# Kernel tuning notes

Measured on AMD Instinct MI355X. Metric: run time of the kernel, lower is better.

The kernel has to match this reference:

```python
import jax, jax.numpy as jnp
import numpy as np

B, C, N, M = 4, 256, 4096, 4096
H, D = 4, 64  # num_heads, head_dim = C // H


def _proj(x, W, b):
    # Conv1d(kernel_size=1): pointwise linear over channel dim. x:(B,Cin,L) W:(Cout,Cin) b:(Cout,)
    return jnp.einsum('oc,bcn->bon', W, x) + b[None, :, None]


def setup_inputs() -> dict:
    key = jax.random.key(0)
    ks = jax.random.split(key, 10)
    s = 1.0 / np.sqrt(C)
    return {
        'query': jax.random.normal(ks[0], (B, C, N), dtype=jnp.float32),
        'source': jax.random.normal(ks[1], (B, C, M), dtype=jnp.float32),
        'Wq': jax.random.normal(ks[2], (C, C), dtype=jnp.float32) * s,
        'bq': jnp.zeros((C,), dtype=jnp.float32),
        'Wk': jax.random.normal(ks[3], (C, C), dtype=jnp.float32) * s,
        'bk': jnp.zeros((C,), dtype=jnp.float32),
        'Wv': jax.random.normal(ks[4], (C, C), dtype=jnp.float32) * s,
        'bv': jnp.zeros((C,), dtype=jnp.float32),
        'Wm': jax.random.normal(ks[5], (C, C), dtype=jnp.float32) * s,
        'bm': jnp.zeros((C,), dtype=jnp.float32),
    }


def reference(query, source, Wq, bq, Wk, bk, Wv, bv, Wm, bm):
    b = query.shape[0]
    n = query.shape[-1]
    Q = _proj(query, Wq, bq).reshape(b, H, D, -1)   # (B,H,D,N)
    K = _proj(source, Wk, bk).reshape(b, H, D, -1)  # (B,H,D,M)
    V = _proj(source, Wv, bv).reshape(b, H, D, -1)  # (B,H,D,M)
    scores = jnp.einsum('bhdn,bhdm->bhnm', Q, K) / (D ** 0.5)
    attn = jax.nn.softmax(scores, axis=-1)
    out = jnp.einsum('bhnm,bhdm->bhdn', attn, V)    # (B,H,D,N)
    out = out.reshape(b, H * D, n)                   # (B,C,N)
    return _proj(out, Wm, bm)
```

## Files before the change

### kernel.cpp

```cpp
#include <hip/hip_runtime.h>
#include <hip/hip_bf16.h>
#include <stdint.h>

#define BB 4
#define CCH 256
#define NN 4096
#define MM 4096
#define HH 4
#define DDIM 64

typedef __attribute__((ext_vector_type(8))) short short8v;
typedef __attribute__((ext_vector_type(4))) float f32x4;
typedef __attribute__((ext_vector_type(16))) float f32x16;

__device__ __forceinline__ unsigned short f2b(float f) {
    unsigned int u = __builtin_bit_cast(unsigned int, f);
    unsigned int r = (u + 0x7FFFu + ((u >> 16) & 1u)) >> 16;
    return (unsigned short)r;
}

__device__ __forceinline__ f32x16 zero16() {
    f32x16 z;
#pragma unroll
    for (int i = 0; i < 16; i++) z[i] = 0.f;
    return z;
}

__global__ __launch_bounds__(256) void convert_kernel(
    const float* __restrict__ q, const float* __restrict__ s,
    const float* __restrict__ Wq, const float* __restrict__ Wk,
    const float* __restrict__ Wv, const float* __restrict__ Wm,
    unsigned short* __restrict__ XTq, unsigned short* __restrict__ XTs,
    unsigned short* __restrict__ Wb) {
    __shared__ float tile[64][65];
    const int bid = blockIdx.x, tid = threadIdx.x;
    if (bid < 2048) {
        const float* in = (bid < 1024) ? q : s;
        unsigned short* out = (bid < 1024) ? XTq : XTs;
        const int r = bid & 1023;
        const int b = r >> 8;
        const int rr = r & 255;
        const int l0 = (rr >> 2) * 64, c0 = (rr & 3) * 64;
#pragma unroll
        for (int i = 0; i < 16; i++) {
            int idx = tid + (i << 8);
            int cc = idx >> 6, ll = idx & 63;
            tile[cc][ll] = in[(size_t)(b * CCH + c0 + cc) * 4096 + l0 + ll];
        }
        __syncthreads();
#pragma unroll
        for (int i = 0; i < 16; i++) {
            int idx = tid + (i << 8);
            int ll = idx >> 6, cc = idx & 63;
            out[((size_t)(b * 4096 + l0 + ll) << 8) + c0 + cc] = f2b(tile[cc][ll]);
        }
    } else {
        const int wid = bid - 2048;
        const int wsel = wid >> 4;
        const float* src = (wsel == 0) ? Wq : (wsel == 1) ? Wk : (wsel == 2) ? Wv : Wm;
        const int off = (wid & 15) * 4096;
#pragma unroll
        for (int i = 0; i < 16; i++) {
            int idx = off + tid + (i << 8);
            Wb[(size_t)wsel * 65536 + idx] = f2b(src[idx]);
        }
    }
}

template <int OUTMODE, bool AHEAD>
__device__ __forceinline__ void gemm_body(const unsigned short* __restrict__ XT,
                                          const unsigned short* __restrict__ W,
                                          const float* __restrict__ bias,
                                          void* __restrict__ outv, float oscale) {
    constexpr int WSTR = 264;
    constexpr int XSTR = 40;
    __shared__ __align__(16) unsigned short Wlds[64 * WSTR];
    __shared__ __align__(16) unsigned short Xlds[256 * XSTR];
    const int tid = threadIdx.x, w = tid >> 6, l = tid & 63;
    const int lg = l >> 4, lm = l & 15;
    const int n0 = blockIdx.x * 256, o0 = blockIdx.y * 64;
    const int oh = (w >> 1) * 32, nh = (w & 1) * 128;

#pragma unroll
    for (int i = 0; i < 8; i++) {
        int idx = tid + (i << 8);
        int row = idx >> 5, c8 = (idx & 31) * 8;
        *(uint4*)&Wlds[row * WSTR + c8] = *(const uint4*)&W[(size_t)(o0 + row) * 256 + c8];
    }

    f32x4 acc[8][2];
#pragma unroll
    for (int nt = 0; nt < 8; nt++)
#pragma unroll
        for (int ot = 0; ot < 2; ot++) acc[nt][ot] = (f32x4){0.f, 0.f, 0.f, 0.f};

    for (int kc = 0; kc < 8; kc++) {
#pragma unroll
        for (int i = 0; i < 4; i++) {
            int idx = tid + (i << 8);
            int row = idx >> 2;
            const unsigned short* srcp;
            if constexpr (AHEAD) {
                int c = kc * 32 + (idx & 3) * 8;
                srcp = XT + ((size_t)(c >> 6) * 4096 + n0 + row) * 64 + (c & 63);
            } else {
                srcp = XT + (size_t)(n0 + row) * 256 + kc * 32 + (idx & 3) * 8;
            }
            *(uint4*)&Xlds[row * XSTR + (idx & 3) * 8] = *(const uint4*)srcp;
        }
        __syncthreads();
        short8v bfrag[2];
#pragma unroll
        for (int ot = 0; ot < 2; ot++)
            bfrag[ot] = *(const short8v*)&Wlds[(oh + ot * 16 + lm) * WSTR + kc * 32 + lg * 8];
#pragma unroll
        for (int nt = 0; nt < 8; nt++) {
            short8v af = *(const short8v*)&Xlds[(nh + nt * 16 + lm) * XSTR + lg * 8];
            acc[nt][0] = __builtin_amdgcn_mfma_f32_16x16x32_bf16(af, bfrag[0], acc[nt][0], 0, 0, 0);
            acc[nt][1] = __builtin_amdgcn_mfma_f32_16x16x32_bf16(af, bfrag[1], acc[nt][1], 0, 0, 0);
        }
        __syncthreads();
    }

#pragma unroll
    for (int nt = 0; nt < 8; nt++)
#pragma unroll
        for (int ot = 0; ot < 2; ot++) {
            int o = o0 + oh + ot * 16 + lm;
            int nb = n0 + nh + nt * 16 + lg * 4;
            float bb = bias[o];
            if constexpr (OUTMODE == 2) {
                float* out = (float*)outv;
                float4 v = make_float4(acc[nt][ot][0] + bb, acc[nt][ot][1] + bb,
                                       acc[nt][ot][2] + bb, acc[nt][ot][3] + bb);
                *(float4*)&out[(size_t)o * 4096 + nb] = v;
            } else if constexpr (OUTMODE == 0) {
                unsigned short* out = (unsigned short*)outv;
                __align__(8) unsigned short v[4];
#pragma unroll
                for (int t = 0; t < 4; t++) v[t] = f2b(acc[nt][ot][t] + bb);
                *(uint2*)&out[(size_t)o * 4096 + nb] = *(uint2*)v;
            } else {
                unsigned short* out = (unsigned short*)outv;
                unsigned short* outp = out + ((size_t)(o >> 6) * 4096 + nb) * 64 + (o & 63);
#pragma unroll
                for (int t = 0; t < 4; t++) outp[t * 64] = f2b((acc[nt][ot][t] + bb) * oscale);
            }
        }
}

__global__ __launch_bounds__(256) void gemm_qkv_kernel(
    const unsigned short* __restrict__ XTq, const unsigned short* __restrict__ XTs,
    const unsigned short* __restrict__ Wb,
    const float* __restrict__ bq, const float* __restrict__ bk, const float* __restrict__ bv,
    unsigned short* __restrict__ QT, unsigned short* __restrict__ KT,
    unsigned short* __restrict__ Vn) {
    const int z = blockIdx.z;
    const int b = z / 3, p = z - b * 3;
    const unsigned short* XT = ((p == 0) ? XTq : XTs) + (size_t)b * 4096 * 256;
    const unsigned short* W = Wb + p * 65536;
    const float* bias = (p == 0) ? bq : (p == 1) ? bk : bv;
    if (p == 2) {
        gemm_body<0, false>(XT, W, bias, Vn + (size_t)b * 256 * 4096, 1.0f);
    } else {
        unsigned short* out = ((p == 0) ? QT : KT) + (size_t)b * 1048576;
        gemm_body<1, false>(XT, W, bias, out, (p == 0) ? 0.1803368801f : 1.0f);
    }
}

__global__ __launch_bounds__(256) void gemm_final_kernel(
    const unsigned short* __restrict__ OH, const unsigned short* __restrict__ Wm,
    const float* __restrict__ bm, float* __restrict__ out) {
    const int b = blockIdx.z;
    gemm_body<2, true>(OH + (size_t)b * 1048576, Wm, bm, out + (size_t)b * 256 * 4096, 1.0f);
}

__device__ __forceinline__ void stage_kv(const unsigned short* __restrict__ Kb,
                                         const unsigned short* __restrict__ Vb,
                                         char* dst, int m0s, int tid) {
    const int rr = tid >> 3, pp = tid & 7;
    const int sw = (pp ^ (rr & 7)) << 4;
    const char* sK = (const char*)(Kb + ((size_t)(m0s + rr) << 6)) + sw;
    const char* sV = (const char*)(Vb + (size_t)rr * 4096 + m0s) + sw;
    __builtin_amdgcn_global_load_lds(
        (const __attribute__((address_space(1))) unsigned int*)sK,
        (__attribute__((address_space(3))) unsigned int*)(dst + (tid << 4)), 16, 0, 0);
    __builtin_amdgcn_global_load_lds(
        (const __attribute__((address_space(1))) unsigned int*)sV,
        (__attribute__((address_space(3))) unsigned int*)(dst + 8192 + (tid << 4)), 16, 0, 0);
}

__global__ __launch_bounds__(512, 2) void attn_kernel(
    const unsigned short* __restrict__ QT, const unsigned short* __restrict__ KT,
    const unsigned short* __restrict__ Vn, unsigned short* __restrict__ OH) {
    __shared__ __align__(16) char smem[32768];
    const int tid = threadIdx.x, w = tid >> 6, l = tid & 63;
    const int lo5 = l & 31, hi = l >> 5;
    const int bh = blockIdx.y, b = bh >> 2, h = bh & 3;
    const int q0 = blockIdx.x * 256 + w * 32;

    short8v qf[4];
    {
        size_t qrow = ((size_t)bh * 4096 + q0 + lo5) * 64;
#pragma unroll
        for (int c = 0; c < 4; c++)
            qf[c] = *(const short8v*)&QT[qrow + c * 16 + hi * 8];
    }

    short8v ones;
#pragma unroll
    for (int j = 0; j < 8; j++) ones[j] = (short)0x3F80;
    f32x16 minit;
#pragma unroll
    for (int r = 0; r < 16; r++) minit[r] = -16.0f;

    const unsigned short* Vb = Vn + ((size_t)b * 256 + h * 64) * 4096;
    const unsigned short* Kb = KT + (size_t)bh * 262144;

    f32x16 o[2];
    o[0] = zero16();
    o[1] = zero16();
    f32x16 sacc = zero16();

    stage_kv(Kb, Vb, smem, 0, tid);

    for (int it = 0; it < 64; it++) {
        __syncthreads();
        char* cur = smem + ((it & 1) << 14);
        if (it < 63) stage_kv(Kb, Vb, smem + (((it + 1) & 1) << 14), (it + 1) * 64, tid);

        short8v kf[2][4];
#pragma unroll
        for (int mc = 0; mc < 2; mc++) {
            int m = mc * 32 + lo5;
#pragma unroll
            for (int c = 0; c < 4; c++)
                kf[mc][c] = *(const short8v*)(cur + m * 128 + (((c * 2 + hi) * 16) ^ ((m & 7) << 4)));
        }
        short8v vf[2][4];
#pragma unroll
        for (int dc = 0; dc < 2; dc++) {
            int d = dc * 32 + lo5;
#pragma unroll
            for (int c = 0; c < 4; c++)
                vf[dc][c] = *(const short8v*)(cur + 8192 + d * 128 + (((c * 2 + hi) * 16) ^ ((d & 7) << 4)));
        }

        f32x16 s[2];
#pragma unroll
        for (int mc = 0; mc < 2; mc++) {
            f32x16 a = __builtin_amdgcn_mfma_f32_32x32x16_bf16(kf[mc][0], qf[0], minit, 0, 0, 0);
#pragma unroll
            for (int c = 1; c < 4; c++)
                a = __builtin_amdgcn_mfma_f32_32x32x16_bf16(kf[mc][c], qf[c], a, 0, 0, 0);
            s[mc] = a;
        }

        short8v pv[2][2];
#pragma unroll
        for (int mc = 0; mc < 2; mc++) {
            float p[16];
#pragma unroll
            for (int r = 0; r < 16; r++) p[r] = exp2f(s[mc][r]);
#pragma unroll
            for (int half = 0; half < 2; half++) {
                union { unsigned int u[4]; short8v v; } pu;
#pragma unroll
                for (int wdx = 0; wdx < 2; wdx++) {
                    unsigned int a, bq;
                    asm("v_cvt_pk_bf16_f32 %0, %1, %2"
                        : "=v"(a) : "v"(p[half * 8 + 2 * wdx]), "v"(p[half * 8 + 2 * wdx + 1]));
                    asm("v_cvt_pk_bf16_f32 %0, %1, %2"
                        : "=v"(bq) : "v"(p[half * 8 + 4 + 2 * wdx]), "v"(p[half * 8 + 4 + 2 * wdx + 1]));
                    asm volatile("v_permlane32_swap_b32 %0, %1" : "+v"(a), "+v"(bq));
                    pu.u[wdx] = a;
                    pu.u[wdx + 2] = bq;
                }
                pv[mc][half] = pu.v;
            }
        }

#pragma unroll
        for (int mc = 0; mc < 2; mc++)
#pragma unroll
            for (int half = 0; half < 2; half++)
                sacc = __builtin_amdgcn_mfma_f32_32x32x16_bf16(ones, pv[mc][half], sacc, 0, 0, 0);

#pragma unroll
        for (int dc = 0; dc < 2; dc++)
#pragma unroll
            for (int mc = 0; mc < 2; mc++)
#pragma unroll
                for (int half = 0; half < 2; half++)
                    o[dc] = __builtin_amdgcn_mfma_f32_32x32x16_bf16(
                        vf[dc][2 * mc + half], pv[mc][half], o[dc], 0, 0, 0);
    }

    float inv = 1.f / sacc[0];
    __syncthreads();
    {
        int row = w * 32 + lo5;
        char* rbase = smem + row * 128;
        int sw = (row & 7) << 4;
#pragma unroll
        for (int dc = 0; dc < 2; dc++)
#pragma unroll
            for (int g = 0; g < 4; g++) {
                ushort4 v4;
                v4.x = f2b(o[dc][g * 4 + 0] * inv);
                v4.y = f2b(o[dc][g * 4 + 1] * inv);
                v4.z = f2b(o[dc][g * 4 + 2] * inv);
                v4.w = f2b(o[dc][g * 4 + 3] * inv);
                int colb = dc * 64 + g * 16 + hi * 8;
                *(ushort4*)(rbase + (colb ^ sw)) = v4;
            }
    }
    __syncthreads();
    {
        int row = tid >> 1, seg = (tid & 1) * 64;
        size_t gbase = ((size_t)bh * 4096 + blockIdx.x * 256 + row) * 64 + (size_t)(tid & 1) * 32;
        int sw = (row & 7) << 4;
#pragma unroll
        for (int ch = 0; ch < 4; ch++) {
            uint4 v = *(const uint4*)(smem + row * 128 + ((seg + ch * 16) ^ sw));
            *(uint4*)&OH[gbase + ch * 8] = v;
        }
    }
}

extern "C" void kernel_launch(void* const* d_in, const int* in_sizes, int n_in,
                              void* d_out, int out_size, void* d_ws, size_t ws_size,
                              hipStream_t stream) {
    const float* q  = (const float*)d_in[0];
    const float* s  = (const float*)d_in[1];
    const float* Wq = (const float*)d_in[2];
    const float* bq = (const float*)d_in[3];
    const float* Wk = (const float*)d_in[4];
    const float* bk = (const float*)d_in[5];
    const float* Wv = (const float*)d_in[6];
    const float* bv = (const float*)d_in[7];
    const float* Wm = (const float*)d_in[8];
    const float* bm = (const float*)d_in[9];
    float* out = (float*)d_out;
    char* ws = (char*)d_ws;

    const size_t SZ = (size_t)BB * 4096 * 256 * 2;
    unsigned short* XTq  = (unsigned short*)(ws);
    unsigned short* XTs  = (unsigned short*)(ws + SZ);
    unsigned short* Wb   = (unsigned short*)(ws + 2 * SZ);
    unsigned short* QT   = (unsigned short*)(ws + 2 * SZ + 524288);
    unsigned short* KTh  = (unsigned short*)(ws + 3 * SZ + 524288);
    unsigned short* Vnat = (unsigned short*)(ws + 4 * SZ + 524288);
    unsigned short* OH   = XTq;

    convert_kernel<<<2112, 256, 0, stream>>>(q, s, Wq, Wk, Wv, Wm, XTq, XTs, Wb);
    gemm_qkv_kernel<<<dim3(16, 4, 12), 256, 0, stream>>>(XTq, XTs, Wb, bq, bk, bv,
                                                         QT, KTh, Vnat);
    attn_kernel<<<dim3(16, 16), 512, 0, stream>>>(QT, KTh, Vnat, OH);
    gemm_final_kernel<<<dim3(16, 4, 4), 256, 0, stream>>>(OH, Wb + 3 * 65536, bm, out);
}
```

Before: 221.3 us.

## Fuse fp32-to-bf16 input transpose into QKV GEMM and reorder attention MFMAs

Drops the separate pass that transposed and converted the query and source activations to bf16. The QKV GEMM now reads fp32 input directly, converts it with packed bf16 instructions, and writes it transposed into LDS. Weight conversion becomes a small vectorized kernel. In the attention loop, K/V fragment offsets are hoisted, the two score chains are interleaved, and s_setprio is placed around the MFMA blocks. The aim is to remove a full activation round trip to memory and improve MFMA issue overlap, at the cost of twice as many input bytes read per GEMM tile. Each input tile is also reloaded by every output-channel block.

```diff
diff --git a/kernel.cpp b/kernel.cpp
--- a/kernel.cpp
+++ b/kernel.cpp
@@ -26,49 +26,22 @@
     return z;
 }
 
-__global__ __launch_bounds__(256) void convert_kernel(
-    const float* __restrict__ q, const float* __restrict__ s,
+__global__ __launch_bounds__(256) void convertW_kernel(
     const float* __restrict__ Wq, const float* __restrict__ Wk,
     const float* __restrict__ Wv, const float* __restrict__ Wm,
-    unsigned short* __restrict__ XTq, unsigned short* __restrict__ XTs,
     unsigned short* __restrict__ Wb) {
-    __shared__ float tile[64][65];
-    const int bid = blockIdx.x, tid = threadIdx.x;
-    if (bid < 2048) {
-        const float* in = (bid < 1024) ? q : s;
-        unsigned short* out = (bid < 1024) ? XTq : XTs;
-        const int r = bid & 1023;
-        const int b = r >> 8;
-        const int rr = r & 255;
-        const int l0 = (rr >> 2) * 64, c0 = (rr & 3) * 64;
-#pragma unroll
-        for (int i = 0; i < 16; i++) {
-            int idx = tid + (i << 8);
-            int cc = idx >> 6, ll = idx & 63;
-            tile[cc][ll] = in[(size_t)(b * CCH + c0 + cc) * 4096 + l0 + ll];
-        }
-        __syncthreads();
-#pragma unroll
-        for (int i = 0; i < 16; i++) {
-            int idx = tid + (i << 8);
-            int ll = idx >> 6, cc = idx & 63;
-            out[((size_t)(b * 4096 + l0 + ll) << 8) + c0 + cc] = f2b(tile[cc][ll]);
-        }
-    } else {
-        const int wid = bid - 2048;
-        const int wsel = wid >> 4;
-        const float* src = (wsel == 0) ? Wq : (wsel == 1) ? Wk : (wsel == 2) ? Wv : Wm;
-        const int off = (wid & 15) * 4096;
-#pragma unroll
-        for (int i = 0; i < 16; i++) {
-            int idx = off + tid + (i << 8);
-            Wb[(size_t)wsel * 65536 + idx] = f2b(src[idx]);
-        }
-    }
-}
-
-template <int OUTMODE, bool AHEAD>
-__device__ __forceinline__ void gemm_body(const unsigned short* __restrict__ XT,
+    const int g = (blockIdx.x << 8) | threadIdx.x;
+    const int wsel = g >> 14;
+    const float* src = (wsel == 0) ? Wq : (wsel == 1) ? Wk : (wsel == 2) ? Wv : Wm;
+    const int off = (g & 16383) * 4;
+    float4 v = *(const float4*)&src[off];
+    ushort4 o;
+    o.x = f2b(v.x); o.y = f2b(v.y); o.z = f2b(v.z); o.w = f2b(v.w);
+    *(ushort4*)&Wb[(size_t)wsel * 65536 + off] = o;
+}
+
+template <int OUTMODE, int INMODE>
+__device__ __forceinline__ void gemm_body(const void* __restrict__ Xv,
                                           const unsigned short* __restrict__ W,
                                           const float* __restrict__ bias,
                                           void* __restrict__ outv, float oscale) {
@@ -95,18 +68,38 @@
         for (int ot = 0; ot < 2; ot++) acc[nt][ot] = (f32x4){0.f, 0.f, 0.f, 0.f};
 
     for (int kc = 0; kc < 8; kc++) {
-#pragma unroll
-        for (int i = 0; i < 4; i++) {
-            int idx = tid + (i << 8);
-            int row = idx >> 2;
-            const unsigned short* srcp;
-            if constexpr (AHEAD) {
+        if constexpr (INMODE == 1) {
+            const float* Xf = (const float*)Xv;
+            const int c4 = (tid & 7) * 4, n8 = (tid >> 3) * 8;
+            float4 rv[4][2];
+#pragma unroll
+            for (int r = 0; r < 4; r++) {
+                const float* rp = Xf + (size_t)(kc * 32 + c4 + r) * 4096 + n0 + n8;
+                rv[r][0] = *(const float4*)rp;
+                rv[r][1] = *(const float4*)(rp + 4);
+            }
+#pragma unroll
+            for (int n = 0; n < 8; n++) {
+                float v0 = ((const float*)&rv[0][n >> 2])[n & 3];
+                float v1 = ((const float*)&rv[1][n >> 2])[n & 3];
+                float v2 = ((const float*)&rv[2][n >> 2])[n & 3];
+                float v3 = ((const float*)&rv[3][n >> 2])[n & 3];
+                unsigned int lo, hi2;
+                asm("v_cvt_pk_bf16_f32 %0, %1, %2" : "=v"(lo) : "v"(v0), "v"(v1));
+                asm("v_cvt_pk_bf16_f32 %0, %1, %2" : "=v"(hi2) : "v"(v2), "v"(v3));
+                *(uint2*)&Xlds[(n8 + n) * XSTR + c4] = make_uint2(lo, hi2);
+            }
+        } else {
+            const unsigned short* XT = (const unsigned short*)Xv;
+#pragma unroll
+            for (int i = 0; i < 4; i++) {
+                int idx = tid + (i << 8);
+                int row = idx >> 2;
                 int c = kc * 32 + (idx & 3) * 8;
-                srcp = XT + ((size_t)(c >> 6) * 4096 + n0 + row) * 64 + (c & 63);
-            } else {
-                srcp = XT + (size_t)(n0 + row) * 256 + kc * 32 + (idx & 3) * 8;
-            }
-            *(uint4*)&Xlds[row * XSTR + (idx & 3) * 8] = *(const uint4*)srcp;
+                const unsigned short* srcp =
+                    XT + ((size_t)(c >> 6) * 4096 + n0 + row) * 64 + (c & 63);
+                *(uint4*)&Xlds[row * XSTR + (idx & 3) * 8] = *(const uint4*)srcp;
+            }
         }
         __syncthreads();
         short8v bfrag[2];
@@ -150,21 +143,21 @@
 }
 
 __global__ __launch_bounds__(256) void gemm_qkv_kernel(
-    const unsigned short* __restrict__ XTq, const unsigned short* __restrict__ XTs,
+    const float* __restrict__ Xq, const float* __restrict__ Xs,
     const unsigned short* __restrict__ Wb,
     const float* __restrict__ bq, const float* __restrict__ bk, const float* __restrict__ bv,
     unsigned short* __restrict__ QT, unsigned short* __restrict__ KT,
     unsigned short* __restrict__ Vn) {
     const int z = blockIdx.z;
     const int b = z / 3, p = z - b * 3;
-    const unsigned short* XT = ((p == 0) ? XTq : XTs) + (size_t)b * 4096 * 256;
+    const float* X = ((p == 0) ? Xq : Xs) + (size_t)b * CCH * 4096;
     const unsigned short* W = Wb + p * 65536;
     const float* bias = (p == 0) ? bq : (p == 1) ? bk : bv;
     if (p == 2) {
-        gemm_body<0, false>(XT, W, bias, Vn + (size_t)b * 256 * 4096, 1.0f);
+        gemm_body<0, 1>(X, W, bias, Vn + (size_t)b * 256 * 4096, 1.0f);
     } else {
         unsigned short* out = ((p == 0) ? QT : KT) + (size_t)b * 1048576;
-        gemm_body<1, false>(XT, W, bias, out, (p == 0) ? 0.1803368801f : 1.0f);
+        gemm_body<1, 1>(X, W, bias, out, (p == 0) ? 0.1803368801f : 1.0f);
     }
 }
 
@@ -172,7 +165,7 @@
     const unsigned short* __restrict__ OH, const unsigned short* __restrict__ Wm,
     const float* __restrict__ bm, float* __restrict__ out) {
     const int b = blockIdx.z;
-    gemm_body<2, true>(OH + (size_t)b * 1048576, Wm, bm, out + (size_t)b * 256 * 4096, 1.0f);
+    gemm_body<2, 2>(OH + (size_t)b * 1048576, Wm, bm, out + (size_t)b * 256 * 4096, 1.0f);
 }
 
 __device__ __forceinline__ void stage_kv(const unsigned short* __restrict__ Kb,
@@ -207,6 +200,15 @@
             qf[c] = *(const short8v*)&QT[qrow + c * 16 + hi * 8];
     }
 
+    int koff[2][4];
+#pragma unroll
+    for (int mc = 0; mc < 2; mc++) {
+        int m = mc * 32 + lo5;
+#pragma unroll
+        for (int c = 0; c < 4; c++)
+            koff[mc][c] = m * 128 + (((c * 2 + hi) * 16) ^ ((m & 7) << 4));
+    }
+
     short8v ones;
 #pragma unroll
     for (int j = 0; j < 8; j++) ones[j] = (short)0x3F80;
@@ -229,39 +231,32 @@
         char* cur = smem + ((it & 1) << 14);
         if (it < 63) stage_kv(Kb, Vb, smem + (((it + 1) & 1) << 14), (it + 1) * 64, tid);
 
-        short8v kf[2][4];
+        short8v kf[2][4], vf[2][4];
+#pragma unroll
+        for (int mc = 0; mc < 2; mc++)
+#pragma unroll
+            for (int c = 0; c < 4; c++) {
+                const char* p = cur + koff[mc][c];
+                kf[mc][c] = *(const short8v*)p;
+                vf[mc][c] = *(const short8v*)(p + 8192);
+            }
+
+        f32x16 s0 = minit, s1 = minit;
+        __builtin_amdgcn_s_setprio(1);
+#pragma unroll
+        for (int c = 0; c < 4; c++) {
+            s0 = __builtin_amdgcn_mfma_f32_32x32x16_bf16(kf[0][c], qf[c], s0, 0, 0, 0);
+            s1 = __builtin_amdgcn_mfma_f32_32x32x16_bf16(kf[1][c], qf[c], s1, 0, 0, 0);
+        }
+        __builtin_amdgcn_s_setprio(0);
+
+        short8v pv[2][2];
 #pragma unroll
         for (int mc = 0; mc < 2; mc++) {
-            int m = mc * 32 + lo5;
-#pragma unroll
-            for (int c = 0; c < 4; c++)
-                kf[mc][c] = *(const short8v*)(cur + m * 128 + (((c * 2 + hi) * 16) ^ ((m & 7) << 4)));
-        }
-        short8v vf[2][4];
-#pragma unroll
-        for (int dc = 0; dc < 2; dc++) {
-            int d = dc * 32 + lo5;
-#pragma unroll
-            for (int c = 0; c < 4; c++)
-                vf[dc][c] = *(const short8v*)(cur + 8192 + d * 128 + (((c * 2 + hi) * 16) ^ ((d & 7) << 4)));
-        }
-
-        f32x16 s[2];
-#pragma unroll
-        for (int mc = 0; mc < 2; mc++) {
-            f32x16 a = __builtin_amdgcn_mfma_f32_32x32x16_bf16(kf[mc][0], qf[0], minit, 0, 0, 0);
-#pragma unroll
-            for (int c = 1; c < 4; c++)
-                a = __builtin_amdgcn_mfma_f32_32x32x16_bf16(kf[mc][c], qf[c], a, 0, 0, 0);
-            s[mc] = a;
-        }
-
-        short8v pv[2][2];
-#pragma unroll
-        for (int mc = 0; mc < 2; mc++) {
+            const f32x16& sm = (mc == 0) ? s0 : s1;
             float p[16];
 #pragma unroll
-            for (int r = 0; r < 16; r++) p[r] = exp2f(s[mc][r]);
+            for (int r = 0; r < 16; r++) p[r] = exp2f(sm[r]);
 #pragma unroll
             for (int half = 0; half < 2; half++) {
                 union { unsigned int u[4]; short8v v; } pu;
@@ -280,20 +275,18 @@
             }
         }
 
+        __builtin_amdgcn_s_setprio(1);
 #pragma unroll
         for (int mc = 0; mc < 2; mc++)
 #pragma unroll
-            for (int half = 0; half < 2; half++)
+            for (int half = 0; half < 2; half++) {
                 sacc = __builtin_amdgcn_mfma_f32_32x32x16_bf16(ones, pv[mc][half], sacc, 0, 0, 0);
-
-#pragma unroll
-        for (int dc = 0; dc < 2; dc++)
-#pragma unroll
-            for (int mc = 0; mc < 2; mc++)
-#pragma unroll
-                for (int half = 0; half < 2; half++)
-                    o[dc] = __builtin_amdgcn_mfma_f32_32x32x16_bf16(
-                        vf[dc][2 * mc + half], pv[mc][half], o[dc], 0, 0, 0);
+                o[0] = __builtin_amdgcn_mfma_f32_32x32x16_bf16(
+                    vf[0][2 * mc + half], pv[mc][half], o[0], 0, 0, 0);
+                o[1] = __builtin_amdgcn_mfma_f32_32x32x16_bf16(
+                    vf[1][2 * mc + half], pv[mc][half], o[1], 0, 0, 0);
+            }
+        __builtin_amdgcn_s_setprio(0);
     }
 
     float inv = 1.f / sacc[0];
@@ -345,16 +338,14 @@
     char* ws = (char*)d_ws;
 
     const size_t SZ = (size_t)BB * 4096 * 256 * 2;
-    unsigned short* XTq  = (unsigned short*)(ws);
-    unsigned short* XTs  = (unsigned short*)(ws + SZ);
-    unsigned short* Wb   = (unsigned short*)(ws + 2 * SZ);
-    unsigned short* QT   = (unsigned short*)(ws + 2 * SZ + 524288);
-    unsigned short* KTh  = (unsigned short*)(ws + 3 * SZ + 524288);
-    unsigned short* Vnat = (unsigned short*)(ws + 4 * SZ + 524288);
-    unsigned short* OH   = XTq;
-
-    convert_kernel<<<2112, 256, 0, stream>>>(q, s, Wq, Wk, Wv, Wm, XTq, XTs, Wb);
-    gemm_qkv_kernel<<<dim3(16, 4, 12), 256, 0, stream>>>(XTq, XTs, Wb, bq, bk, bv,
+    unsigned short* Wb   = (unsigned short*)(ws);
+    unsigned short* QT   = (unsigned short*)(ws + 524288);
+    unsigned short* KTh  = (unsigned short*)(ws + 524288 + SZ);
+    unsigned short* Vnat = (unsigned short*)(ws + 524288 + 2 * SZ);
+    unsigned short* OH   = (unsigned short*)(ws + 524288 + 3 * SZ);
+
+    convertW_kernel<<<256, 256, 0, stream>>>(Wq, Wk, Wv, Wm, Wb);
+    gemm_qkv_kernel<<<dim3(16, 4, 12), 256, 0, stream>>>(q, s, Wb, bq, bk, bv,
                                                          QT, KTh, Vnat);
     attn_kernel<<<dim3(16, 16), 512, 0, stream>>>(QT, KTh, Vnat, OH);
     gemm_final_kernel<<<dim3(16, 4, 4), 256, 0, stream>>>(OH, Wb + 3 * 65536, bm, out);
```

Result: slower. 252.2 us (+14.0%).
